# Performance work log

Measured on AMD Instinct MI355X. Metric: run time of the kernel, lower is better.

Reference implementation:

```python
import jax, jax.numpy as jnp
import numpy as np

T, B, I, H = 1024, 256, 256, 256
SIGMA = 0.01


def setup_inputs() -> dict:
    key = jax.random.key(0)
    k1, k2, k3 = jax.random.split(key, 3)
    inputs = jax.random.normal(k1, (T, B, I), dtype=jnp.float32)
    W_xh = jax.random.normal(k2, (I, H), dtype=jnp.float32) * SIGMA
    W_hh = jax.random.normal(k3, (H, H), dtype=jnp.float32) * SIGMA
    b_h = jnp.zeros((H,), dtype=jnp.float32)
    return {"inputs": inputs, "W_xh": W_xh, "W_hh": W_hh, "b_h": b_h}


def reference(inputs, W_xh, W_hh, b_h):
    # inputs: [T, B, I]; initial state zeros([B, H]) as in the torch module.
    state0 = jnp.zeros((inputs.shape[1], W_hh.shape[0]), dtype=inputs.dtype)

    def step(state, x_t):
        new_state = jnp.tanh(x_t @ W_xh + state @ W_hh + b_h)
        return new_state, new_state

    state, outputs = jax.lax.scan(step, state0, inputs)
    # outputs: [T, B, H] (stacked per-timestep hidden states), state: [B, H]
    return outputs, state
```

## Files before the change

### kernel.cpp

```cpp
#include <hip/hip_runtime.h>


#define TT 1024
#define BB 256
#define HH 256

typedef __attribute__((ext_vector_type(8))) _Float16 f16x8;
typedef __attribute__((ext_vector_type(4))) float f32x4;

__global__ __launch_bounds__(256, 2) void xw_gemm_f16(const float* __restrict__ X,
                                                      const float* __restrict__ W,
                                                      const float* __restrict__ bh,
                                                      float* __restrict__ out) {
    const int tid  = threadIdx.x;
    const int lane = tid & 63;
    const int wave = tid >> 6;
    const int c    = lane & 15;
    const int quad = lane >> 4;

    f16x8 bf[4][8];
#pragma unroll
    for (int nt = 0; nt < 4; nt++) {
        const int n = wave * 64 + nt * 16 + c;
#pragma unroll
        for (int kt = 0; kt < 8; kt++) {
            const int kb = kt * 32 + quad * 8;
            f16x8 v;
#pragma unroll
            for (int j = 0; j < 8; j++)
                v[j] = (_Float16)W[(size_t)(kb + j) * HH + n];
            bf[nt][kt] = v;
        }
    }
    float bb[4];
#pragma unroll
    for (int nt = 0; nt < 4; nt++) bb[nt] = bh[wave * 64 + nt * 16 + c];

    const int ntiles = (TT * BB) / 16;
    for (int tile = blockIdx.x; tile < ntiles; tile += gridDim.x) {
        const float* xp = X + ((size_t)tile * 16 + c) * 256 + quad * 8;
        f16x8 af[8];
#pragma unroll
        for (int kt = 0; kt < 8; kt++) {
            float4 lo = *(const float4*)(xp + kt * 32);
            float4 hi = *(const float4*)(xp + kt * 32 + 4);
            f16x8 v;
            v[0] = (_Float16)lo.x; v[1] = (_Float16)lo.y;
            v[2] = (_Float16)lo.z; v[3] = (_Float16)lo.w;
            v[4] = (_Float16)hi.x; v[5] = (_Float16)hi.y;
            v[6] = (_Float16)hi.z; v[7] = (_Float16)hi.w;
            af[kt] = v;
        }

        f32x4 acc[4];
#pragma unroll
        for (int nt = 0; nt < 4; nt++) acc[nt] = (f32x4){0.f, 0.f, 0.f, 0.f};
#pragma unroll
        for (int kt = 0; kt < 8; kt++)
#pragma unroll
            for (int nt = 0; nt < 4; nt++)
                acc[nt] = __builtin_amdgcn_mfma_f32_16x16x32_f16(af[kt], bf[nt][kt], acc[nt], 0, 0, 0);

        const size_t rbase = (size_t)tile * 16 + quad * 4;
#pragma unroll
        for (int nt = 0; nt < 4; nt++) {
            const int col = wave * 64 + nt * 16 + c;
#pragma unroll
            for (int i = 0; i < 4; i++)
                out[(rbase + i) * 256 + col] = acc[nt][i] + bb[nt];
        }
    }
}

__device__ __forceinline__ float fast_tanh(float x) {
    float e = __expf(2.0f * x);
    return 1.0f - 2.0f * __builtin_amdgcn_rcpf(e + 1.0f);
}

#define SP 272

#define STEP(T, XW, CUR, NXT)                                                     \
    {                                                                             \
        f16x8 af[8];                                                              \
        if (realrow) {                                                            \
            _Pragma("unroll")                                                     \
            for (int kt = 0; kt < 8; kt++)                                        \
                af[kt] = *(const f16x8*)&st[CUR][r][kt * 32 + quad * 8];          \
        } else {                                                                  \
            _Pragma("unroll")                                                     \
            for (int kt = 0; kt < 8; kt++) af[kt] = (f16x8)(_Float16)0.f;         \
        }                                                                         \
        f32x4 accE[4], accO[4];                                                   \
        _Pragma("unroll")                                                         \
        for (int nt = 0; nt < 4; nt++) {                                          \
            accE[nt] = (f32x4){XW[nt], 0.f, 0.f, 0.f};                            \
            accO[nt] = (f32x4){0.f, 0.f, 0.f, 0.f};                               \
        }                                                                         \
         \
        {                                                                         \
            const int tp = ((T) + 2 > TT - 1) ? (TT - 1) : ((T) + 2);             \
            _Pragma("unroll")                                                     \
            for (int nt = 0; nt < 4; nt++)                                        \
                XW[nt] = out[(size_t)tp * (BB * HH) + colbase + nt * 16];         \
        }                                                                         \
        _Pragma("unroll")                                                         \
        for (int kt = 0; kt < 4; kt++)                                            \
            _Pragma("unroll")                                                     \
            for (int nt = 0; nt < 4; nt++) {                                      \
                accE[nt] = __builtin_amdgcn_mfma_f32_16x16x32_f16(af[2 * kt], bf[nt][2 * kt], accE[nt], 0, 0, 0); \
                accO[nt] = __builtin_amdgcn_mfma_f32_16x16x32_f16(af[2 * kt + 1], bf[nt][2 * kt + 1], accO[nt], 0, 0, 0); \
            }                                                                     \
        const size_t obase = (size_t)(T) * (BB * HH) + colbase;                   \
        _Pragma("unroll")                                                         \
        for (int nt = 0; nt < 4; nt++) {                                          \
            h[nt] = fast_tanh(accE[nt][0] + accO[nt][0]);                         \
            out[obase + nt * 16] = h[nt];                                         \
            st[NXT][quad][wave * 64 + nt * 16 + c] = (_Float16)h[nt];             \
        }                                                                         \
          \
        asm volatile("s_waitcnt lgkmcnt(0)" ::: "memory");                        \
        __builtin_amdgcn_s_barrier();                                             \
        __builtin_amdgcn_sched_barrier(0);                                        \
    }

__global__ __launch_bounds__(256, 1) void rnn_rec_mfma(const float* __restrict__ Whh,
                                                       float* __restrict__ out) {
    __shared__ alignas(16) _Float16 st[2][4][SP];

    const int tid  = threadIdx.x;
    const int lane = tid & 63;
    const int wave = tid >> 6;
    const int c    = lane & 15;
    const int quad = lane >> 4;
    const int b0   = blockIdx.x * 4;

    f16x8 bf[4][8];
#pragma unroll
    for (int nt = 0; nt < 4; nt++) {
        const int n = wave * 64 + nt * 16 + c;
#pragma unroll
        for (int kt = 0; kt < 8; kt++) {
            const int kb = kt * 32 + quad * 8;
            f16x8 v;
#pragma unroll
            for (int j = 0; j < 8; j++)
                v[j] = (_Float16)Whh[(size_t)(kb + j) * HH + n];
            bf[nt][kt] = v;
        }
    }

    for (int i = tid; i < 2 * 4 * SP; i += 256)
        ((_Float16*)st)[i] = (_Float16)0.f;

    const int  m       = c;
    const bool realrow = ((m & 3) == 0);
    const int  r       = m >> 2;

    const size_t colbase = (size_t)(b0 + quad) * HH + wave * 64 + c;
    float xwA[4], xwB[4];
#pragma unroll
    for (int nt = 0; nt < 4; nt++) xwA[nt] = out[colbase + nt * 16];
#pragma unroll
    for (int nt = 0; nt < 4; nt++) xwB[nt] = out[(size_t)BB * HH + colbase + nt * 16];

    asm volatile("s_waitcnt lgkmcnt(0)" ::: "memory");
    __builtin_amdgcn_s_barrier();
    __builtin_amdgcn_sched_barrier(0);

    float h[4] = {0.f, 0.f, 0.f, 0.f};

#pragma unroll 1
    for (int t = 0; t < TT; t += 2) {
        STEP(t,     xwA, 0, 1)
        STEP(t + 1, xwB, 1, 0)
    }

    const size_t fbase = (size_t)TT * (BB * HH) + colbase;
#pragma unroll
    for (int nt = 0; nt < 4; nt++) out[fbase + nt * 16] = h[nt];
}

extern "C" void kernel_launch(void* const* d_in, const int* in_sizes, int n_in,
                              void* d_out, int out_size, void* d_ws, size_t ws_size,
                              hipStream_t stream) {
    const float* X   = (const float*)d_in[0];
    const float* Wxh = (const float*)d_in[1];
    const float* Whh = (const float*)d_in[2];
    const float* bh  = (const float*)d_in[3];
    float* out = (float*)d_out;

    xw_gemm_f16<<<dim3(1024), dim3(256), 0, stream>>>(X, Wxh, bh, out);
    rnn_rec_mfma<<<dim3(BB / 4), dim3(256), 0, stream>>>(Whh, out);
}
```

Measured before the change: 1.166 ms.

## Stage input projection as packed fp16 workspace for recurrence prefetch

The input-projection GEMM now writes its result in fp16 to a workspace, with columns permuted so each recurrence lane fetches its four needed values in one 8-byte load instead of four scattered fp32 loads. The GEMM grid is split over two column halves with 2048 row-blocks to raise parallelism. The recurrence drops the realrow branch and always reads shared state. This cuts global traffic and latency on the sequential critical path, at the cost of fp16 rounding of the projection. The old fp32 path remains as a fallback when no workspace is available.

```diff
diff --git a/kernel.cpp b/kernel.cpp
--- a/kernel.cpp
+++ b/kernel.cpp
@@ -6,22 +6,33 @@
 #define HH 256
 
 typedef __attribute__((ext_vector_type(8))) _Float16 f16x8;
+typedef __attribute__((ext_vector_type(4))) _Float16 f16x4;
+typedef __attribute__((ext_vector_type(2))) _Float16 f16x2;
 typedef __attribute__((ext_vector_type(4))) float f32x4;
 
-__global__ __launch_bounds__(256, 2) void xw_gemm_f16(const float* __restrict__ X,
-                                                      const float* __restrict__ W,
-                                                      const float* __restrict__ bh,
-                                                      float* __restrict__ out) {
+__device__ __forceinline__ float fast_tanh(float x) {
+    float e = __expf(2.0f * x);
+    return 1.0f - 2.0f * __builtin_amdgcn_rcpf(e + 1.0f);
+}
+
+template <bool TOWS>
+__global__ __launch_bounds__(256, 2) void xw_gemm(const float* __restrict__ X,
+                                                  const float* __restrict__ W,
+                                                  const float* __restrict__ bh,
+                                                  _Float16* __restrict__ ws,
+                                                  float* __restrict__ out) {
     const int tid  = threadIdx.x;
     const int lane = tid & 63;
     const int wave = tid >> 6;
     const int c    = lane & 15;
     const int quad = lane >> 4;
-
-    f16x8 bf[4][8];
-#pragma unroll
-    for (int nt = 0; nt < 4; nt++) {
-        const int n = wave * 64 + nt * 16 + c;
+    const int hf   = blockIdx.y;
+    const int nb   = hf * 128 + wave * 32;
+
+    f16x8 bfx[2][8];
+#pragma unroll
+    for (int nt = 0; nt < 2; nt++) {
+        const int n = nb + nt * 16 + c;
 #pragma unroll
         for (int kt = 0; kt < 8; kt++) {
             const int kb = kt * 32 + quad * 8;
@@ -29,16 +40,16 @@
 #pragma unroll
             for (int j = 0; j < 8; j++)
                 v[j] = (_Float16)W[(size_t)(kb + j) * HH + n];
-            bf[nt][kt] = v;
-        }
-    }
-    float bb[4];
-#pragma unroll
-    for (int nt = 0; nt < 4; nt++) bb[nt] = bh[wave * 64 + nt * 16 + c];
+            bfx[nt][kt] = v;
+        }
+    }
+    float bb[2];
+#pragma unroll
+    for (int nt = 0; nt < 2; nt++) bb[nt] = bh[nb + nt * 16 + c];
 
     const int ntiles = (TT * BB) / 16;
-    for (int tile = blockIdx.x; tile < ntiles; tile += gridDim.x) {
-        const float* xp = X + ((size_t)tile * 16 + c) * 256 + quad * 8;
+    for (int rt = blockIdx.x; rt < ntiles; rt += gridDim.x) {
+        const float* xp = X + ((size_t)rt * 16 + c) * HH + quad * 8;
         f16x8 af[8];
 #pragma unroll
         for (int kt = 0; kt < 8; kt++) {
@@ -52,62 +63,69 @@
             af[kt] = v;
         }
 
-        f32x4 acc[4];
-#pragma unroll
-        for (int nt = 0; nt < 4; nt++) acc[nt] = (f32x4){0.f, 0.f, 0.f, 0.f};
+        f32x4 acc[2];
+#pragma unroll
+        for (int nt = 0; nt < 2; nt++) acc[nt] = (f32x4){0.f, 0.f, 0.f, 0.f};
 #pragma unroll
         for (int kt = 0; kt < 8; kt++)
 #pragma unroll
-            for (int nt = 0; nt < 4; nt++)
-                acc[nt] = __builtin_amdgcn_mfma_f32_16x16x32_f16(af[kt], bf[nt][kt], acc[nt], 0, 0, 0);
-
-        const size_t rbase = (size_t)tile * 16 + quad * 4;
-#pragma unroll
-        for (int nt = 0; nt < 4; nt++) {
-            const int col = wave * 64 + nt * 16 + c;
-#pragma unroll
-            for (int i = 0; i < 4; i++)
-                out[(rbase + i) * 256 + col] = acc[nt][i] + bb[nt];
-        }
-    }
-}
-
-__device__ __forceinline__ float fast_tanh(float x) {
-    float e = __expf(2.0f * x);
-    return 1.0f - 2.0f * __builtin_amdgcn_rcpf(e + 1.0f);
+            for (int nt = 0; nt < 2; nt++)
+                acc[nt] = __builtin_amdgcn_mfma_f32_16x16x32_f16(af[kt], bfx[nt][kt], acc[nt], 0, 0, 0);
+
+        if (TOWS) {
+            const int pbase = (hf * 2 + (wave >> 1)) * 64 + c * 4 + (wave & 1) * 2;
+#pragma unroll
+            for (int i = 0; i < 4; i++) {
+                const size_t R = (size_t)rt * 16 + quad * 4 + i;
+                f16x2 v;
+                v[0] = (_Float16)(acc[0][i] + bb[0]);
+                v[1] = (_Float16)(acc[1][i] + bb[1]);
+                *(f16x2*)(ws + R * HH + pbase) = v;
+            }
+        } else {
+#pragma unroll
+            for (int i = 0; i < 4; i++) {
+                const size_t R = (size_t)rt * 16 + quad * 4 + i;
+#pragma unroll
+                for (int nt = 0; nt < 2; nt++)
+                    out[R * HH + nb + nt * 16 + c] = acc[nt][i] + bb[nt];
+            }
+        }
+    }
 }
 
 #define SP 272
 
-#define STEP(T, XW, CUR, NXT)                                                     \
+#define STEP(T, XWH, XWF, CUR, NXT)                                               \
     {                                                                             \
-        f16x8 af[8];                                                              \
-        if (realrow) {                                                            \
-            _Pragma("unroll")                                                     \
-            for (int kt = 0; kt < 8; kt++)                                        \
-                af[kt] = *(const f16x8*)&st[CUR][r][kt * 32 + quad * 8];          \
-        } else {                                                                  \
-            _Pragma("unroll")                                                     \
-            for (int kt = 0; kt < 8; kt++) af[kt] = (f16x8)(_Float16)0.f;         \
-        }                                                                         \
+        f16x8 af[8];             \
+        _Pragma("unroll")                                                         \
+        for (int kt = 0; kt < 8; kt++)                                            \
+            af[kt] = *(const f16x8*)&st[CUR][r][kt * 32 + quad * 8];              \
         f32x4 accE[4], accO[4];                                                   \
         _Pragma("unroll")                                                         \
         for (int nt = 0; nt < 4; nt++) {                                          \
-            accE[nt] = (f32x4){XW[nt], 0.f, 0.f, 0.f};                            \
+            float xv;                                                             \
+            if constexpr (FROMWS) xv = (float)XWH[nt]; else xv = XWF[nt];         \
+            accE[nt] = (f32x4){xv, 0.f, 0.f, 0.f};                                \
             accO[nt] = (f32x4){0.f, 0.f, 0.f, 0.f};                               \
         }                                                                         \
-         \
+                 \
         {                                                                         \
             const int tp = ((T) + 2 > TT - 1) ? (TT - 1) : ((T) + 2);             \
-            _Pragma("unroll")                                                     \
-            for (int nt = 0; nt < 4; nt++)                                        \
-                XW[nt] = out[(size_t)tp * (BB * HH) + colbase + nt * 16];         \
+            if constexpr (FROMWS) {                                               \
+                XWH = *(const f16x4*)(ws + (size_t)tp * (BB * HH) + wsoff);       \
+            } else {                                                              \
+                _Pragma("unroll")                                                 \
+                for (int nt = 0; nt < 4; nt++)                                    \
+                    XWF[nt] = out[(size_t)tp * (BB * HH) + colbase + nt * 16];    \
+            }                                                                     \
         }                                                                         \
         _Pragma("unroll")                                                         \
         for (int kt = 0; kt < 4; kt++)                                            \
             _Pragma("unroll")                                                     \
             for (int nt = 0; nt < 4; nt++) {                                      \
-                accE[nt] = __builtin_amdgcn_mfma_f32_16x16x32_f16(af[2 * kt], bf[nt][2 * kt], accE[nt], 0, 0, 0); \
+                accE[nt] = __builtin_amdgcn_mfma_f32_16x16x32_f16(af[2 * kt],     bf[nt][2 * kt],     accE[nt], 0, 0, 0); \
                 accO[nt] = __builtin_amdgcn_mfma_f32_16x16x32_f16(af[2 * kt + 1], bf[nt][2 * kt + 1], accO[nt], 0, 0, 0); \
             }                                                                     \
         const size_t obase = (size_t)(T) * (BB * HH) + colbase;                   \
@@ -117,13 +135,14 @@
             out[obase + nt * 16] = h[nt];                                         \
             st[NXT][quad][wave * 64 + nt * 16 + c] = (_Float16)h[nt];             \
         }                                                                         \
-          \
         asm volatile("s_waitcnt lgkmcnt(0)" ::: "memory");                        \
         __builtin_amdgcn_s_barrier();                                             \
         __builtin_amdgcn_sched_barrier(0);                                        \
     }
 
+template <bool FROMWS>
 __global__ __launch_bounds__(256, 1) void rnn_rec_mfma(const float* __restrict__ Whh,
+                                                       const _Float16* __restrict__ ws,
                                                        float* __restrict__ out) {
     __shared__ alignas(16) _Float16 st[2][4][SP];
 
@@ -152,16 +171,22 @@
     for (int i = tid; i < 2 * 4 * SP; i += 256)
         ((_Float16*)st)[i] = (_Float16)0.f;
 
-    const int  m       = c;
-    const bool realrow = ((m & 3) == 0);
-    const int  r       = m >> 2;
+    const int r = c >> 2;
 
     const size_t colbase = (size_t)(b0 + quad) * HH + wave * 64 + c;
-    float xwA[4], xwB[4];
-#pragma unroll
-    for (int nt = 0; nt < 4; nt++) xwA[nt] = out[colbase + nt * 16];
-#pragma unroll
-    for (int nt = 0; nt < 4; nt++) xwB[nt] = out[(size_t)BB * HH + colbase + nt * 16];
+    const size_t wsoff   = (size_t)(b0 + quad) * HH + wave * 64 + c * 4;
+
+    f16x4 xwhA, xwhB;
+    float xwfA[4], xwfB[4];
+    if constexpr (FROMWS) {
+        xwhA = *(const f16x4*)(ws + wsoff);
+        xwhB = *(const f16x4*)(ws + (size_t)BB * HH + wsoff);
+    } else {
+#pragma unroll
+        for (int nt = 0; nt < 4; nt++) xwfA[nt] = out[colbase + nt * 16];
+#pragma unroll
+        for (int nt = 0; nt < 4; nt++) xwfB[nt] = out[(size_t)BB * HH + colbase + nt * 16];
+    }
 
     asm volatile("s_waitcnt lgkmcnt(0)" ::: "memory");
     __builtin_amdgcn_s_barrier();
@@ -171,8 +196,8 @@
 
 #pragma unroll 1
     for (int t = 0; t < TT; t += 2) {
-        STEP(t,     xwA, 0, 1)
-        STEP(t + 1, xwB, 1, 0)
+        STEP(t,     xwhA, xwfA, 0, 1)
+        STEP(t + 1, xwhB, xwfB, 1, 0)
     }
 
     const size_t fbase = (size_t)TT * (BB * HH) + colbase;
@@ -189,6 +214,13 @@
     const float* bh  = (const float*)d_in[3];
     float* out = (float*)d_out;
 
-    xw_gemm_f16<<<dim3(1024), dim3(256), 0, stream>>>(X, Wxh, bh, out);
-    rnn_rec_mfma<<<dim3(BB / 4), dim3(256), 0, stream>>>(Whh, out);
-}
+    const size_t need = (size_t)TT * BB * HH * sizeof(_Float16);
+    if (d_ws != nullptr && ws_size >= need) {
+        _Float16* ws = (_Float16*)d_ws;
+        xw_gemm<true><<<dim3(2048, 2), dim3(256), 0, stream>>>(X, Wxh, bh, ws, out);
+        rnn_rec_mfma<true><<<dim3(BB / 4), dim3(256), 0, stream>>>(Whh, ws, out);
+    } else {
+        xw_gemm<false><<<dim3(2048, 2), dim3(256), 0, stream>>>(X, Wxh, bh, nullptr, out);
+        rnn_rec_mfma<false><<<dim3(BB / 4), dim3(256), 0, stream>>>(Whh, nullptr, out);
+    }
+}
```

Result: faster. 1.132 ms (-3.0%).
